# Performance work log

Measured on AMD Instinct MI355X. Metric: run time of the kernel, lower is better.

The kernel has to match this reference:

```python
import jax, jax.numpy as jnp
import numpy as np

K = 10          # neighbors per span
KTOK = 3        # heads used per span
D = 2.0         # token adjacency threshold
GAMMA = 1.0
MAX_WIDTH = 16
CAP = 128       # cap_spans_per_token
B, L, KTOK_TOTAL = 8, 128, 4


def _enumerate_spans(L, max_width):
    ar = np.arange(L)
    l_g, r_g = np.meshgrid(ar, ar, indexing='ij')
    mask = (r_g >= l_g) & (r_g - l_g + 1 <= max_width)
    l_idx = l_g[mask]
    r_idx = r_g[mask]
    S = l_idx.size
    span2id = np.full((L, L), -1, dtype=np.int64)
    span2id[l_idx, r_idx] = np.arange(S)
    return span2id, l_idx, r_idx, S


def _geom_matrix(L, max_width, span2id, l_idx, r_idx):
    # 8-neighborhood (l+/-1, r+/-1) adjacency over span ids, boolean (S,S)
    S = l_idx.size
    off = np.array([[-1, -1], [-1, 0], [-1, 1], [0, -1], [0, 1], [1, -1], [1, 0], [1, 1]])
    nl = l_idx[:, None] + off[None, :, 0]
    nr = r_idx[:, None] + off[None, :, 1]
    valid = (nl >= 0) & (nr >= 0) & (nl <= nr) & (nr < L) & (nr - nl + 1 <= max_width)
    s2 = span2id[np.clip(nl, 0, L - 1), np.clip(nr, 0, L - 1)]
    rows = np.broadcast_to(np.arange(S)[:, None], s2.shape)
    m = valid & (s2 >= 0)
    Geom = np.zeros((S, S), dtype=bool)
    Geom[rows[m], s2[m]] = True
    np.fill_diagonal(Geom, False)
    return Geom


SPAN2ID, L_IDX, R_IDX, S = _enumerate_spans(L, MAX_WIDTH)
GEOM = jnp.asarray(_geom_matrix(L, MAX_WIDTH, SPAN2ID, L_IDX, R_IDX))


def setup_inputs() -> dict:
    key = jax.random.key(0)
    k1, k2, k3 = jax.random.split(key, 3)
    head_indices = jax.random.randint(k1, (B, L, L, KTOK_TOTAL), 0, L)
    head_weights = jax.random.uniform(k2, (B, L, L, KTOK_TOTAL), dtype=jnp.float32)
    dist = jax.random.uniform(k3, (B, L, L), dtype=jnp.float32) * 8.0
    return {"head_indices": head_indices, "head_weights": head_weights, "dist": dist}


def reference(head_indices, head_weights, dist):
    l_idx = jnp.asarray(L_IDX)
    r_idx = jnp.asarray(R_IDX)
    # gather per-span head indices/weights: (B, S, Ktok)
    idx_all = head_indices[:, l_idx, r_idx, :KTOK]
    w_all = head_weights[:, l_idx, r_idx, :KTOK]
    valid1 = idx_all >= 0
    idx_safe = jnp.clip(idx_all, 0, None)
    w_all = w_all * valid1.astype(w_all.dtype)

    # scatter-add token->span dense matrices: (B, S, L)
    b_ix = jnp.arange(B)[:, None, None]
    s_ix = jnp.arange(S)[None, :, None]
    P_w = jnp.zeros((B, S, L), w_all.dtype).at[b_ix, s_ix, idx_safe].add(w_all)
    P_bin = jnp.zeros((B, S, L), jnp.float32).at[b_ix, s_ix, idx_safe].add(valid1.astype(jnp.float32))

    # token adjacency with self loops
    A = jnp.maximum((dist <= D).astype(jnp.float32), jnp.eye(L, dtype=jnp.float32))
    U_mask = jnp.einsum('bsl,blm->bsm', P_bin, A) > 0.0  # (B, S, L) spans hitting token m

    # top-1 head token -> span one-hot, with per-token span cap
    top1 = jnp.clip(idx_all[:, :, 0], 0, L - 1)
    top1_valid = (idx_all[:, :, 0] >= 0).astype(jnp.float32)
    E = jax.nn.one_hot(top1, L, dtype=jnp.float32) * top1_valid[..., None]  # (B, S, L)
    E = jnp.swapaxes(E, 1, 2)  # (B, L, S)
    E = E * (jnp.cumsum(E, axis=2) <= float(CAP)).astype(jnp.float32)

    # candidate matrix M: (B, S, S)
    M = jnp.einsum('bsl,blt->bst', U_mask.astype(jnp.float32), E) > 0.0
    diag = jnp.arange(S)
    M = M.at[:, diag, diag].set(False)
    M = M | GEOM[None]

    # gate scores Gate = P_w @ exp(-gamma*dist) @ P_w^T
    G = jnp.exp(-GAMMA * dist)
    A_pw = jnp.einsum('bsl,blm->bsm', P_w, G)
    Gate = jnp.einsum('bsm,btm->bst', A_pw, P_w)

    Gate_masked = jnp.where(M, Gate, -jnp.inf)
    topk_vals, topk_idx = jax.lax.top_k(Gate_masked, K)  # (B, S, K)
    N_mask = jnp.isfinite(topk_vals)
    N_idx = topk_idx.astype(jnp.int32)

    # self-loop fill for invalid slots
    rows = jnp.broadcast_to(jnp.arange(S, dtype=N_idx.dtype)[None, :, None], (B, S, K))
    N_idx = jnp.where(N_mask, N_idx, rows)
    N_mask = jnp.ones_like(N_mask)
    return N_idx, N_mask
```

## Files before the change

kernel.cpp:

```cpp
#include <hip/hip_runtime.h>
#include <stdint.h>

#define NB 8
#define LL 128
#define NS 1928
#define NK 10
#define WPB 4
#define SPW 4
#define SLOTS 32

__device__ __forceinline__ int span_id(int l, int r) {
    int off = (l <= 112) ? (l << 4) : (NS - (((128 - l) * (129 - l)) >> 1));
    return off + (r - l);
}

__device__ __forceinline__ float npexp_f32(float x) {
    const float magic = 12582912.0f;
    const float log2e = 1.442695040888963f;
    const float c1 = -6.93145752e-1f;
    const float c2 = -1.42860677e-6f;
    float t = __fmul_rn(x, log2e);
    float q = __fsub_rn(__fadd_rn(t, magic), magic);
    float r = __fmaf_rn(q, c1, x);
    r = __fmaf_rn(q, c2, r);
    float num = __fmaf_rn(r, 5.082762527590693718096e-04f, 6.757896990527504603057e-03f);
    num = __fmaf_rn(num, r, 5.114512081637298353406e-02f);
    num = __fmaf_rn(num, r, 2.473615434895520810817e-01f);
    num = __fmaf_rn(num, r, 7.257664613233124478488e-01f);
    num = __fmaf_rn(num, r, 9.999999999980870924916e-01f);
    float den = __fmaf_rn(r, 2.159509375685829852307e-02f, -2.742335390411667452936e-01f);
    den = __fmaf_rn(den, r, 1.0f);
    float p = __fdiv_rn(num, den);
    int qi = (int)q;
    return __fmul_rn(p, __int_as_float((127 + qi) << 23));
}

__device__ __forceinline__ float keyval(unsigned long long k) {
    return __uint_as_float((unsigned)(k >> 32));
}

__device__ __forceinline__ float f4c(const float4& v, int x) {
    return x == 0 ? v.x : (x == 1 ? v.y : (x == 2 ? v.z : v.w));
}

__device__ __forceinline__ void wfence() {
    __builtin_amdgcn_wave_barrier();
    __threadfence_block();
    __builtin_amdgcn_wave_barrier();
}

__device__ int wave_partition_fast(unsigned long long* a, int* posL, int* posR,
                                   int pl, int pr, int lane) {
    int pm = pl + ((pr - pl) >> 1);
    unsigned long long vl = a[pl], vm = a[pm], vr = a[pr], tt;
    if (keyval(vm) < keyval(vl)) { tt = vm; vm = vl; vl = tt; }
    if (keyval(vr) < keyval(vm)) { tt = vr; vr = vm; vm = tt; }
    if (keyval(vm) < keyval(vl)) { tt = vm; vm = vl; vl = tt; }
    float vp = keyval(vm);
    unsigned long long vq = a[pr - 1];
    if (lane == 0) { a[pl] = vl; a[pr] = vr; a[pm] = vq; a[pr - 1] = vm; }
    wfence();

    unsigned long long lmask = (1ull << lane) - 1ull;
    int baseL = 0, baseR = 0;
    for (int p0 = pl; p0 <= pr; p0 += 64) {
        int pos = p0 + lane;
        bool inr = (pos <= pr);
        float v = inr ? keyval(a[pos]) : 0.0f;
        bool ge = inr && (pos > pl) && (pos < pr) && (v >= vp);
        bool le = inr && (pos <= pr - 2) && (v <= vp);
        unsigned long long bge = __ballot(ge);
        unsigned long long ble = __ballot(le);
        if (ge) posL[baseL + __popcll(bge & lmask)] = pos;
        if (le) posR[baseR + __popcll(ble & lmask)] = pos;
        baseL += __popcll(bge);
        baseR += __popcll(ble);
    }
    wfence();
    int totGE = baseL, totLE = baseR;
    int maxk = (totGE < totLE) ? totGE : totLE;
    int K = 0;
    for (int base = 0;; base += 64) {
        int k = base + lane;
        bool active = (k < maxk);
        int Lk = active ? posL[k] : 0x7fffffff;
        int Rk = active ? posR[totLE - 1 - k] : -1;
        bool sw = active && (Lk < Rk);
        unsigned long long bm = __ballot(sw);
        int nsw = (~bm == 0ull) ? 64 : (__ffsll((long long)~bm) - 1);
        if (sw && (lane < nsw)) {
            unsigned long long tl = a[Lk], tr = a[Rk];
            a[Lk] = tr; a[Rk] = tl;
        }
        K += nsw;
        if (nsw < 64) break;
    }
    wfence();
    int pi = posL[K];
    if (K > 0) { int rp = posR[totLE - K]; if (rp < pi) pi = rp; }
    if (lane == 0) { tt = a[pi]; a[pi] = a[pr - 1]; a[pr - 1] = tt; }
    wfence();
    return pi;
}

__device__ __forceinline__ void lane_sift(unsigned long long* h, int start, int hm) {
    unsigned long long tmp = h[start];
    int i = start, j = start + start;
    while (j <= hm) {
        if (j < hm && keyval(h[j]) < keyval(h[j + 1])) ++j;
        if (keyval(tmp) < keyval(h[j])) { h[i] = h[j]; i = j; j += j; }
        else break;
    }
    h[i] = tmp;
}

__device__ void wave_heap_top(unsigned long long* a, int lo, int hi, int needlo, int lane) {
    unsigned long long* h = a + lo - 1;
    int hm = hi - lo + 1;
    int half = hm >> 1;
    int maxlvl = 0; { int v = half; while (v >>= 1) ++maxlvl; }
    for (int lvl = maxlvl; lvl >= 0; --lvl) {
        int n0 = 1 << lvl;
        int n1 = (n0 << 1) - 1; if (n1 > half) n1 = half;
        for (int nb = n0; nb <= n1; nb += 64) {
            int node = nb + lane;
            if (node <= n1) lane_sift(h, node, hm);
        }
        wfence();
    }
    int E = hi - needlo + 1;
    if (E > hm - 1) E = hm - 1;
    if (lane == 0) {
        int m = hm;
        for (int e = 0; e < E; ++e) {
            unsigned long long tmp = h[m]; h[m] = h[1]; --m;
            int i = 1, j = 2;
            while (j <= m) {
                if (j < m && keyval(h[j]) < keyval(h[j + 1])) ++j;
                if (keyval(tmp) < keyval(h[j])) { h[i] = h[j]; i = j; j += j; }
                else break;
            }
            h[i] = tmp;
        }
    }
    wfence();
}

__device__ void wave_insertion(unsigned long long* a, int lo, int hi, int lane) {
    int len = hi - lo + 1;
    unsigned long long v = (lane < len) ? a[lo + lane] : 0ull;
    float fv = keyval(v);
    int rank = 0;
    for (int j = 0; j < len; ++j) {
        unsigned long long vj = __shfl(v, j, 64);
        float fj = keyval(vj);
        if ((fj < fv) || (fj == fv && j < lane)) ++rank;
    }
    wfence();
    if (lane < len) a[lo + rank] = v;
    wfence();
}

__device__ void wave_np_sort_top(unsigned long long* a, int n, int lane, int* stk,
                                 int* posL, int* posR) {
    int depth = 0; { int v = n; while (v >>= 1) ++depth; }
    depth *= 2;
    const int TOPLO = n - NK;
    int sp = 0;
    int lo = 0, hi = n - 1;
    for (;;) {
        while (hi - lo > 15) {
            if (depth-- < 0) {
                if (hi >= TOPLO) wave_heap_top(a, lo, hi, (lo > TOPLO ? lo : TOPLO), lane);
                goto pop;
            }
            {
                int pi = wave_partition_fast(a, posL, posR, lo, hi, lane);
                if (pi - lo < hi - pi) {
                    if (lane == 0) { stk[sp * 2] = pi + 1; stk[sp * 2 + 1] = hi; }
                    ++sp; hi = pi - 1;
                } else {
                    if (lane == 0) { stk[sp * 2] = lo; stk[sp * 2 + 1] = pi - 1; }
                    ++sp; lo = pi + 1;
                }
                wfence();
            }
        }
        if (hi > lo && hi >= TOPLO) wave_insertion(a, lo, hi, lane);
pop:
        if (sp == 0) break;
        --sp;
        lo = stk[sp * 2]; hi = stk[sp * 2 + 1];
    }
}

__global__ __launch_bounds__(256)
void build_tables_kernel(const int* __restrict__ hi, const float* __restrict__ hw,
                         float4* __restrict__ g_pack, uint16_t* __restrict__ g_lrc,
                         unsigned char* __restrict__ top1) {
    int j = blockIdx.x * 256 + threadIdx.x;
    if (j >= NB * LL * 16) return;
    int b = j >> 11;
    int lw = j & 2047;
    int l = lw >> 4, w = lw & 15, r = l + w;
    if (r >= LL) return;
    int sid = span_id(l, r);
    const int* hb = hi + b * LL * LL * 4;
    const float* wb = hw + b * LL * LL * 4;
    int4 iv = *(const int4*)(hb + (l * LL + r) * 4);
    float4 wv = *(const float4*)(wb + (l * LL + r) * 4);
    int ia = iv.x, ib = iv.y, ic = iv.z;
    float wa = wv.x, wb2 = wv.y, wc = wv.z;
    int m0, m1 = 255, m2 = 255;
    float W0, W1 = 0.f, W2 = 0.f;
    if (ia == ib && ib == ic) {
        m0 = ia; W0 = __fadd_rn(__fadd_rn(wa, wb2), wc);
    } else if (ia == ib) {
        float W = __fadd_rn(wa, wb2);
        if (ia < ic) { m0 = ia; W0 = W; m1 = ic; W1 = wc; }
        else         { m0 = ic; W0 = wc; m1 = ia; W1 = W; }
    } else if (ia == ic) {
        float W = __fadd_rn(wa, wc);
        if (ia < ib) { m0 = ia; W0 = W; m1 = ib; W1 = wb2; }
        else         { m0 = ib; W0 = wb2; m1 = ia; W1 = W; }
    } else if (ib == ic) {
        float W = __fadd_rn(wb2, wc);
        if (ia < ib) { m0 = ia; W0 = wa; m1 = ib; W1 = W; }
        else         { m0 = ib; W0 = W; m1 = ia; W1 = wa; }
    } else {
        int x0 = ia, x1 = ib, x2 = ic; float y0 = wa, y1 = wb2, y2 = wc;
        if (x0 > x1) { int tx = x0; x0 = x1; x1 = tx; float ty = y0; y0 = y1; y1 = ty; }
        if (x1 > x2) { int tx = x1; x1 = x2; x2 = tx; float ty = y1; y1 = y2; y2 = ty; }
        if (x0 > x1) { int tx = x0; x0 = x1; x1 = tx; float ty = y0; y0 = y1; y1 = ty; }
        m0 = x0; m1 = x1; m2 = x2; W0 = y0; W1 = y1; W2 = y2;
    }
    uint32_t rec = (uint32_t)m0 | ((uint32_t)m1 << 8) | ((uint32_t)m2 << 16)
                 | ((uint32_t)(ia & 127) << 24);
    g_pack[b * NS + sid] = make_float4(W0, W1, W2, __uint_as_float(rec));
    g_lrc[b * NS + sid] = (uint16_t)(l | (r << 7));
    top1[b * NS + sid] = (unsigned char)(ia & 127);
}

__global__ void cap_kernel(const unsigned char* __restrict__ top1,
                           unsigned char* __restrict__ flags) {
    int gw = (blockIdx.x * blockDim.x + threadIdx.x) >> 6;
    int lane = threadIdx.x & 63;
    int b = gw >> 7, l = gw & 127;
    const unsigned char* tb = top1 + b * NS;
    unsigned char* fb = flags + b * NS;
    int cnt = 0;
    for (int t0 = 0; t0 < NS; t0 += 64) {
        int t = t0 + lane;
        int tp = (t < NS) ? (int)tb[t] : 255;
        bool match = (tp == l);
        unsigned long long m = __ballot(match);
        if (match) {
            int pre = __popcll(m & ((1ull << lane) - 1ull));
            fb[t] = (cnt + pre + 1 <= 128) ? 1 : 0;
        }
        cnt += __popcll(m);
    }
}

__device__ __forceinline__ void load_tables(const float4* __restrict__ gp,
                                            const uint16_t* __restrict__ gl,
                                            const unsigned char* __restrict__ fb,
                                            float4* s_pack, uint16_t* s_lrc) {
    for (int j = threadIdx.x; j < NS; j += 256) {
        float4 v = gp[j];
        uint32_t rec = __float_as_uint(v.w) | ((uint32_t)(fb[j] & 1) << 31);
        v.w = __uint_as_float(rec);
        s_pack[j] = v;
        s_lrc[j] = gl[j];
    }
}

__device__ __forceinline__ void span_prologue(const float* __restrict__ db, float4 ps,
                                              int lane, float* qrow, int stride,
                                              unsigned long long* ub) {
    uint32_t rec = __float_as_uint(ps.w);
    int m0 = rec & 255, m1 = (rec >> 8) & 255, m2 = (rec >> 16) & 255;
    bool e1 = (m1 != 255), e2 = (m2 != 255);
    const float* row0 = db + m0 * LL;
    const float* row1 = db + (e1 ? m1 : 0) * LL;
    const float* row2 = db + (e2 ? m2 : 0) * LL;
    int mA = lane, mB = lane + 64;
    float dA0 = row0[mA], dB0 = row0[mB];
    float dA1 = row1[mA], dB1 = row1[mB];
    float dA2 = row2[mA], dB2 = row2[mB];
    float qA = __fmaf_rn(ps.x, npexp_f32(-dA0), 0.0f);
    qA = __fmaf_rn(ps.y, npexp_f32(-dA1), qA);
    qA = __fmaf_rn(ps.z, npexp_f32(-dA2), qA);
    float qB = __fmaf_rn(ps.x, npexp_f32(-dB0), 0.0f);
    qB = __fmaf_rn(ps.y, npexp_f32(-dB1), qB);
    qB = __fmaf_rn(ps.z, npexp_f32(-dB2), qB);
    bool cA = (dA0 <= 2.0f || mA == m0) ||
              (e1 && (dA1 <= 2.0f || mA == m1)) ||
              (e2 && (dA2 <= 2.0f || mA == m2));
    bool cB = (dB0 <= 2.0f || mB == m0) ||
              (e1 && (dB1 <= 2.0f || mB == m1)) ||
              (e2 && (dB2 <= 2.0f || mB == m2));
    ub[0] = __ballot(cA);
    ub[1] = __ballot(cB);
    qrow[mA * stride] = qA;
    qrow[mB * stride] = qB;
}

__device__ __forceinline__ void topk_merge(unsigned key, int t0, int lane,
                                           unsigned& v, int& vi, unsigned& tau) {
    unsigned long long bm = __ballot(key > tau);
    while (bm) {
        int ln = __ffsll((long long)bm) - 1;
        bm &= bm - 1;
        unsigned kk = (unsigned)__builtin_amdgcn_readlane((int)key, ln);
        if (kk > tau) {
            int tk = t0 + ln;
            unsigned vprev = (unsigned)__builtin_amdgcn_update_dpp(
                -1, (int)v, 0x138 , 0xF, 0xF, false);
            int iprev = __builtin_amdgcn_update_dpp(
                0, vi, 0x138 , 0xF, 0xF, false);
            bool keep = (v >= kk);
            bool fp = (vprev < kk);
            v = keep ? v : (fp ? vprev : kk);
            vi = keep ? vi : (fp ? iprev : tk);
            tau = (unsigned)__builtin_amdgcn_readlane((int)v, 10);
        }
    }
}

__device__ __forceinline__ void topk_merge_idx(unsigned key, int tval,
                                               unsigned& v, int& vi, unsigned& tau) {
    unsigned long long bm = __ballot(key > tau);
    while (bm) {
        int ln = __ffsll((long long)bm) - 1;
        bm &= bm - 1;
        unsigned kk = (unsigned)__builtin_amdgcn_readlane((int)key, ln);
        if (kk > tau) {
            int tk = __builtin_amdgcn_readlane(tval, ln);
            unsigned vprev = (unsigned)__builtin_amdgcn_update_dpp(
                -1, (int)v, 0x138, 0xF, 0xF, false);
            int iprev = __builtin_amdgcn_update_dpp(
                0, vi, 0x138, 0xF, 0xF, false);
            bool keep = (v >= kk);
            bool fp = (vprev < kk);
            v = keep ? v : (fp ? vprev : kk);
            vi = keep ? vi : (fp ? iprev : tk);
            tau = (unsigned)__builtin_amdgcn_readlane((int)v, 10);
        }
    }
}

__device__ __forceinline__ void span_epilogue(unsigned v, int vi, int b, int s, int lane,
                                              unsigned char* __restrict__ rowflag,
                                              int* __restrict__ out) {
    unsigned vn = __shfl_down(v, 1, 64);
    bool tie = (lane < NK) && (v != 0u) && (vn == v);
    bool flag = (__ballot(tie) != 0ull);
    if (lane < NK) {
        int o = (b * NS + s) * NK + lane;
        out[NB * NS * NK + o] = 1;
        if (!flag) out[o] = (vi >= 0) ? vi : s;
    }
    if (lane == 0) rowflag[b * NS + s] = flag ? 1 : 0;
}

__global__ __launch_bounds__(256)
void span_scan_kernel(const float4* __restrict__ g_pack,
                      const uint16_t* __restrict__ g_lrc,
                      const float* __restrict__ dist,
                      const unsigned char* __restrict__ capf,
                      unsigned char* __restrict__ rowflag,
                      int* __restrict__ out) {
    __shared__ float4 s_pack[NS];
    __shared__ float4 s_q4[WPB][LL];

    const int b = blockIdx.y;
    {
        const float4* gp = g_pack + b * NS;
        const unsigned char* fb = capf + b * NS;
        for (int j = threadIdx.x; j < NS; j += 256) {
            float4 v = gp[j];
            v.w = __uint_as_float(__float_as_uint(v.w) | ((uint32_t)(fb[j] & 1) << 31));
            s_pack[j] = v;
        }
    }
    __syncthreads();

    const int wid = threadIdx.x >> 6;
    const int lane = threadIdx.x & 63;
    const int base = blockIdx.x * (WPB * SPW);
    const float* db = dist + b * LL * LL;
    const uint16_t* glb = g_lrc + b * NS;

    int ss[SPW]; bool ok[SPW]; int schunk[SPW];
    int lsv[SPW], rsv[SPW];
    unsigned long long ub0[SPW], ub1[SPW];

    #pragma unroll
    for (int x = 0; x < SPW; ++x) {
        int s = base + x * WPB + wid;
        ok[x] = (s < NS);
        s = ok[x] ? s : 0;
        ss[x] = s;
        schunk[x] = s & ~63;
        uint32_t lrc = glb[s];
        lsv[x] = lrc & 127;
        rsv[x] = (lrc >> 7) & 127;
        unsigned long long ub[2];
        span_prologue(db, s_pack[s], lane, (float*)&s_q4[wid][0] + x, 4, ub);
        ub0[x] = ub[0]; ub1[x] = ub[1];
    }
    const float4* qq = s_q4[wid];

    unsigned v[SPW] = {0u, 0u, 0u, 0u};
    int vi[SPW] = {-1, -1, -1, -1};
    unsigned tau[SPW] = {0u, 0u, 0u, 0u};

    const int NCH = (NS + 63) >> 6;

    float4 ptc = s_pack[lane];
    uint32_t rtc = __float_as_uint(ptc.w);
    float4 q0 = qq[rtc & 127];
    float4 q1 = qq[(rtc >> 8) & 127];
    float4 q2 = qq[(rtc >> 16) & 127];

    for (int c = 0; c < NCH; ++c) {
        const int t0 = c << 6;
        const int t = t0 + lane;
        const bool inr = (t < NS);
        const bool hasnext = (c + 1 < NCH);

        float4 ptn = ptc;
        {
            int tn = t0 + 64 + lane;
            if (tn > NS - 1) tn = NS - 1;
            if (hasnext) ptn = s_pack[tn];
        }

        unsigned key[SPW];
        {
            int sh = (int)((rtc >> 24) & 63);
            bool hi2 = ((rtc >> 24) & 64) != 0;
            bool cum = ((int)rtc) < 0;
            #pragma unroll
            for (int x = 0; x < SPW; ++x) {
                float g = __fmaf_rn(ptc.x, f4c(q0, x), 0.0f);
                g = __fmaf_rn(ptc.y, f4c(q1, x), g);
                g = __fmaf_rn(ptc.z, f4c(q2, x), g);
                unsigned long long bits = hi2 ? ub1[x] : ub0[x];
                bool um = (((bits >> sh) & 1ull) != 0) && cum && inr;
                key[x] = um ? __float_as_uint(g) : 0u;
            }
            #pragma unroll
            for (int x = 0; x < SPW; ++x)
                if (t0 == schunk[x]) key[x] = (t == ss[x]) ? 0u : key[x];
        }

        uint32_t rtn = rtc;
        float4 n0 = q0, n1 = q1, n2 = q2;
        if (hasnext) {
            rtn = __float_as_uint(ptn.w);
            n0 = qq[rtn & 127];
            n1 = qq[(rtn >> 8) & 127];
            n2 = qq[(rtn >> 16) & 127];
        }

        #pragma unroll
        for (int x = 0; x < SPW; ++x)
            topk_merge(key[x], t0, lane, v[x], vi[x], tau[x]);

        ptc = ptn; rtc = rtn; q0 = n0; q1 = n1; q2 = n2;
    }

    {
        int j = lane + (lane >= 4 ? 1 : 0);
        int dl = j / 3 - 1, dr = j % 3 - 1;
        #pragma unroll
        for (int x = 0; x < SPW; ++x) {
            int nl = lsv[x] + dl, nr = rsv[x] + dr;
            bool valid = (lane < 8) && (nl >= 0) && (nr >= nl) && (nr < LL)
                         && (nr - nl < 16);
            int tg = valid ? span_id(nl, nr) : 0;
            float4 pt = s_pack[tg];
            uint32_t rt = __float_as_uint(pt.w);
            float g = __fmaf_rn(pt.x, f4c(qq[rt & 127], x), 0.0f);
            g = __fmaf_rn(pt.y, f4c(qq[(rt >> 8) & 127], x), g);
            g = __fmaf_rn(pt.z, f4c(qq[(rt >> 16) & 127], x), g);
            int rb = (int)(rt >> 24);
            unsigned long long bits = (rb & 64) ? ub1[x] : ub0[x];
            bool um = (((bits >> (rb & 63)) & 1ull) != 0) && (((int)rt) < 0);
            unsigned key = (valid && !um) ? __float_as_uint(g) : 0u;
            topk_merge_idx(key, tg, v[x], vi[x], tau[x]);
        }
    }

    #pragma unroll
    for (int x = 0; x < SPW; ++x)
        if (ok[x]) span_epilogue(v[x], vi[x], b, ss[x], lane, rowflag, out);
}

__global__ __launch_bounds__(256)
void span_slow_kernel(const float4* __restrict__ g_pack,
                      const uint16_t* __restrict__ g_lrc,
                      const float* __restrict__ dist,
                      const unsigned char* __restrict__ capf,
                      const unsigned char* __restrict__ rowflag,
                      int* __restrict__ out) {
    __shared__ int s_nrows;
    __shared__ int s_rows[64];
    __shared__ float4 s_pack[NS];
    __shared__ uint16_t s_lrc[NS];
    __shared__ float s_qq[LL];
    __shared__ unsigned long long s_cov[2];
    __shared__ unsigned long long s_buf[NS];
    __shared__ int s_posL[NS], s_posR[NS];
    __shared__ int s_stk[48];

    const int b = blockIdx.x;
    const int slot = blockIdx.y;
    const unsigned char* rf = rowflag + b * NS;

    if (threadIdx.x < 64) {
        int lane = threadIdx.x;
        int i = slot + lane * SLOTS;
        bool f = (i < NS) && (rf[i] != 0);
        unsigned long long m = __ballot(f);
        if (f) s_rows[__popcll(m & ((1ull << lane) - 1ull))] = i;
        if (lane == 0) s_nrows = __popcll(m);
    }
    __syncthreads();
    int nrows = s_nrows;
    if (nrows == 0) return;

    load_tables(g_pack + b * NS, g_lrc + b * NS, capf + b * NS, s_pack, s_lrc);
    __syncthreads();

    const int wid = threadIdx.x >> 6;
    const int lane = threadIdx.x & 63;
    const float* db = dist + b * LL * LL;

    for (int ri = 0; ri < nrows; ++ri) {
        const int s = s_rows[ri];
        uint32_t lrc = s_lrc[s];
        int ls = lrc & 127, rs = (lrc >> 7) & 127;

        if (wid == 0) {
            unsigned long long ub[2];
            span_prologue(db, s_pack[s], lane, s_qq, 1, ub);
            if (lane == 0) { s_cov[0] = ub[0]; s_cov[1] = ub[1]; }
        }
        __syncthreads();
        unsigned long long ub0 = s_cov[0], ub1 = s_cov[1];

        for (int t = threadIdx.x; t < NS; t += 256) {
            float4 pt = s_pack[t];
            uint32_t rt = __float_as_uint(pt.w);
            float g = __fmaf_rn(pt.x, s_qq[rt & 127], 0.0f);
            g = __fmaf_rn(pt.y, s_qq[(rt >> 8) & 127], g);
            g = __fmaf_rn(pt.z, s_qq[(rt >> 16) & 127], g);
            uint32_t lr = s_lrc[t];
            int lt = lr & 127, rt2 = (lr >> 7) & 127;
            int dl = lt - ls; if (dl < 0) dl = -dl;
            int dr = rt2 - rs; if (dr < 0) dr = -dr;
            bool neq = (t != s);
            bool geom = neq && (dl <= 1) && (dr <= 1);
            int rb = (int)(rt >> 24);
            unsigned long long bits = (rb & 64) ? ub1 : ub0;
            bool um = (((bits >> (rb & 63)) & 1ull) != 0) && (((int)rt) < 0) && neq;
            unsigned h32 = (um || geom) ? __float_as_uint(g) : 0xFF800000u;
            s_buf[t] = ((unsigned long long)h32 << 32) | (unsigned)t;
        }
        __syncthreads();

        if (wid == 0) {
            wave_np_sort_top(s_buf, NS, lane, s_stk, s_posL, s_posR);
            if (lane < NK) {
                unsigned long long k = s_buf[NS - 1 - lane];
                int idx = ((unsigned)(k >> 32) == 0xFF800000u) ? s : (int)(k & 0xffffffffull);
                out[(b * NS + s) * NK + lane] = idx;
            }
        }
        __syncthreads();
    }
}

extern "C" void kernel_launch(void* const* d_in, const int* in_sizes, int n_in,
                              void* d_out, int out_size, void* d_ws, size_t ws_size,
                              hipStream_t stream) {
    const int* hi = (const int*)d_in[0];
    const float* hw = (const float*)d_in[1];
    const float* dist = (const float*)d_in[2];
    int* out = (int*)d_out;

    unsigned char* ws = (unsigned char*)d_ws;
    unsigned char* top1 = ws;
    unsigned char* capf = ws + NB * NS;
    unsigned char* rowflag = ws + 2 * NB * NS;
    float4* g_pack = (float4*)(ws + 3 * NB * NS);
    uint16_t* g_lrc = (uint16_t*)(ws + 3 * NB * NS + NB * NS * 16);

    build_tables_kernel<<<(NB * LL * 16) / 256, 256, 0, stream>>>(hi, hw, g_pack, g_lrc, top1);
    cap_kernel<<<(NB * LL * 64) / 256, 256, 0, stream>>>(top1, capf);
    dim3 grid((NS + WPB * SPW - 1) / (WPB * SPW), NB);
    span_scan_kernel<<<grid, 256, 0, stream>>>(g_pack, g_lrc, dist, capf, rowflag, out);
    dim3 sgrid(NB, SLOTS);
    span_slow_kernel<<<sgrid, 256, 0, stream>>>(g_pack, g_lrc, dist, capf, rowflag, out);
}
```

Baseline: 193.4 us.

## Fold cap flag into packed table and drop shared-memory staging in scan kernel

The cap kernel now sets the cap bit directly in the packed span table instead of writing a separate flag array. This removes the per-block merge of that array. The scan kernel no longer stages the whole packed table into LDS; it reads it from global memory (L1/L2-cached) and keeps only a smaller per-wave query buffer. Spans per wave drop from 4 to 2, doubling the block count, and bounds checks are removed because NS divides evenly by 8. The trade-off is more global or cache gathers in the inner loop and less reuse of each block's table load across spans.

```diff
diff --git a/kernel.cpp b/kernel.cpp
--- a/kernel.cpp
+++ b/kernel.cpp
@@ -6,7 +6,7 @@
 #define NS 1928
 #define NK 10
 #define WPB 4
-#define SPW 4
+#define SPW 2
 #define SLOTS 32
 
 __device__ __forceinline__ int span_id(int l, int r) {
@@ -39,8 +39,8 @@
     return __uint_as_float((unsigned)(k >> 32));
 }
 
-__device__ __forceinline__ float f4c(const float4& v, int x) {
-    return x == 0 ? v.x : (x == 1 ? v.y : (x == 2 ? v.z : v.w));
+__device__ __forceinline__ float f2c(const float2& v, int x) {
+    return x == 0 ? v.x : v.y;
 }
 
 __device__ __forceinline__ void wfence() {
@@ -242,21 +242,21 @@
 }
 
 __global__ void cap_kernel(const unsigned char* __restrict__ top1,
-                           unsigned char* __restrict__ flags) {
+                           float4* __restrict__ g_pack) {
     int gw = (blockIdx.x * blockDim.x + threadIdx.x) >> 6;
     int lane = threadIdx.x & 63;
     int b = gw >> 7, l = gw & 127;
     const unsigned char* tb = top1 + b * NS;
-    unsigned char* fb = flags + b * NS;
+    uint32_t* gw4 = (uint32_t*)(g_pack + b * NS);
     int cnt = 0;
     for (int t0 = 0; t0 < NS; t0 += 64) {
         int t = t0 + lane;
         int tp = (t < NS) ? (int)tb[t] : 255;
         bool match = (tp == l);
         unsigned long long m = __ballot(match);
-        if (match) {
-            int pre = __popcll(m & ((1ull << lane) - 1ull));
-            fb[t] = (cnt + pre + 1 <= 128) ? 1 : 0;
+        if (match && (cnt + __popcll(m & ((1ull << lane) - 1ull)) + 1 <= 128)) {
+            uint32_t* p = gw4 + t * 4 + 3;
+            *p |= 0x80000000u;
         }
         cnt += __popcll(m);
     }
@@ -264,13 +264,9 @@
 
 __device__ __forceinline__ void load_tables(const float4* __restrict__ gp,
                                             const uint16_t* __restrict__ gl,
-                                            const unsigned char* __restrict__ fb,
                                             float4* s_pack, uint16_t* s_lrc) {
     for (int j = threadIdx.x; j < NS; j += 256) {
-        float4 v = gp[j];
-        uint32_t rec = __float_as_uint(v.w) | ((uint32_t)(fb[j] & 1) << 31);
-        v.w = __uint_as_float(rec);
-        s_pack[j] = v;
+        s_pack[j] = gp[j];
         s_lrc[j] = gl[j];
     }
 }
@@ -368,61 +364,49 @@
 void span_scan_kernel(const float4* __restrict__ g_pack,
                       const uint16_t* __restrict__ g_lrc,
                       const float* __restrict__ dist,
-                      const unsigned char* __restrict__ capf,
                       unsigned char* __restrict__ rowflag,
                       int* __restrict__ out) {
-    __shared__ float4 s_pack[NS];
-    __shared__ float4 s_q4[WPB][LL];
+    __shared__ float2 s_q2[WPB][LL];
 
     const int b = blockIdx.y;
-    {
-        const float4* gp = g_pack + b * NS;
-        const unsigned char* fb = capf + b * NS;
-        for (int j = threadIdx.x; j < NS; j += 256) {
-            float4 v = gp[j];
-            v.w = __uint_as_float(__float_as_uint(v.w) | ((uint32_t)(fb[j] & 1) << 31));
-            s_pack[j] = v;
-        }
-    }
-    __syncthreads();
+    const float4* __restrict__ gpb = g_pack + b * NS;
+    const uint16_t* __restrict__ glb = g_lrc + b * NS;
+    const float* db = dist + b * LL * LL;
 
     const int wid = threadIdx.x >> 6;
     const int lane = threadIdx.x & 63;
     const int base = blockIdx.x * (WPB * SPW);
-    const float* db = dist + b * LL * LL;
-    const uint16_t* glb = g_lrc + b * NS;
-
-    int ss[SPW]; bool ok[SPW]; int schunk[SPW];
+
+    int ss[SPW]; int schunk[SPW];
     int lsv[SPW], rsv[SPW];
     unsigned long long ub0[SPW], ub1[SPW];
 
     #pragma unroll
     for (int x = 0; x < SPW; ++x) {
         int s = base + x * WPB + wid;
-        ok[x] = (s < NS);
-        s = ok[x] ? s : 0;
         ss[x] = s;
         schunk[x] = s & ~63;
         uint32_t lrc = glb[s];
         lsv[x] = lrc & 127;
         rsv[x] = (lrc >> 7) & 127;
         unsigned long long ub[2];
-        span_prologue(db, s_pack[s], lane, (float*)&s_q4[wid][0] + x, 4, ub);
+        span_prologue(db, gpb[s], lane, (float*)&s_q2[wid][0].x + x, 2, ub);
         ub0[x] = ub[0]; ub1[x] = ub[1];
     }
-    const float4* qq = s_q4[wid];
-
-    unsigned v[SPW] = {0u, 0u, 0u, 0u};
-    int vi[SPW] = {-1, -1, -1, -1};
-    unsigned tau[SPW] = {0u, 0u, 0u, 0u};
+    __syncthreads();
+    const float2* qq = s_q2[wid];
+
+    unsigned v[SPW] = {0u, 0u};
+    int vi[SPW] = {-1, -1};
+    unsigned tau[SPW] = {0u, 0u};
 
     const int NCH = (NS + 63) >> 6;
 
-    float4 ptc = s_pack[lane];
+    float4 ptc = gpb[lane];
     uint32_t rtc = __float_as_uint(ptc.w);
-    float4 q0 = qq[rtc & 127];
-    float4 q1 = qq[(rtc >> 8) & 127];
-    float4 q2 = qq[(rtc >> 16) & 127];
+    float2 q0 = qq[rtc & 127];
+    float2 q1 = qq[(rtc >> 8) & 127];
+    float2 q2 = qq[(rtc >> 16) & 127];
 
     for (int c = 0; c < NCH; ++c) {
         const int t0 = c << 6;
@@ -434,7 +418,7 @@
         {
             int tn = t0 + 64 + lane;
             if (tn > NS - 1) tn = NS - 1;
-            if (hasnext) ptn = s_pack[tn];
+            if (hasnext) ptn = gpb[tn];
         }
 
         unsigned key[SPW];
@@ -444,9 +428,9 @@
             bool cum = ((int)rtc) < 0;
             #pragma unroll
             for (int x = 0; x < SPW; ++x) {
-                float g = __fmaf_rn(ptc.x, f4c(q0, x), 0.0f);
-                g = __fmaf_rn(ptc.y, f4c(q1, x), g);
-                g = __fmaf_rn(ptc.z, f4c(q2, x), g);
+                float g = __fmaf_rn(ptc.x, f2c(q0, x), 0.0f);
+                g = __fmaf_rn(ptc.y, f2c(q1, x), g);
+                g = __fmaf_rn(ptc.z, f2c(q2, x), g);
                 unsigned long long bits = hi2 ? ub1[x] : ub0[x];
                 bool um = (((bits >> sh) & 1ull) != 0) && cum && inr;
                 key[x] = um ? __float_as_uint(g) : 0u;
@@ -457,7 +441,7 @@
         }
 
         uint32_t rtn = rtc;
-        float4 n0 = q0, n1 = q1, n2 = q2;
+        float2 n0 = q0, n1 = q1, n2 = q2;
         if (hasnext) {
             rtn = __float_as_uint(ptn.w);
             n0 = qq[rtn & 127];
@@ -481,11 +465,11 @@
             bool valid = (lane < 8) && (nl >= 0) && (nr >= nl) && (nr < LL)
                          && (nr - nl < 16);
             int tg = valid ? span_id(nl, nr) : 0;
-            float4 pt = s_pack[tg];
+            float4 pt = gpb[tg];
             uint32_t rt = __float_as_uint(pt.w);
-            float g = __fmaf_rn(pt.x, f4c(qq[rt & 127], x), 0.0f);
-            g = __fmaf_rn(pt.y, f4c(qq[(rt >> 8) & 127], x), g);
-            g = __fmaf_rn(pt.z, f4c(qq[(rt >> 16) & 127], x), g);
+            float g = __fmaf_rn(pt.x, f2c(qq[rt & 127], x), 0.0f);
+            g = __fmaf_rn(pt.y, f2c(qq[(rt >> 8) & 127], x), g);
+            g = __fmaf_rn(pt.z, f2c(qq[(rt >> 16) & 127], x), g);
             int rb = (int)(rt >> 24);
             unsigned long long bits = (rb & 64) ? ub1[x] : ub0[x];
             bool um = (((bits >> (rb & 63)) & 1ull) != 0) && (((int)rt) < 0);
@@ -496,14 +480,13 @@
 
     #pragma unroll
     for (int x = 0; x < SPW; ++x)
-        if (ok[x]) span_epilogue(v[x], vi[x], b, ss[x], lane, rowflag, out);
+        span_epilogue(v[x], vi[x], b, ss[x], lane, rowflag, out);
 }
 
 __global__ __launch_bounds__(256)
 void span_slow_kernel(const float4* __restrict__ g_pack,
                       const uint16_t* __restrict__ g_lrc,
                       const float* __restrict__ dist,
-                      const unsigned char* __restrict__ capf,
                       const unsigned char* __restrict__ rowflag,
                       int* __restrict__ out) {
     __shared__ int s_nrows;
@@ -532,7 +515,7 @@
     int nrows = s_nrows;
     if (nrows == 0) return;
 
-    load_tables(g_pack + b * NS, g_lrc + b * NS, capf + b * NS, s_pack, s_lrc);
+    load_tables(g_pack + b * NS, g_lrc + b * NS, s_pack, s_lrc);
     __syncthreads();
 
     const int wid = threadIdx.x >> 6;
@@ -594,15 +577,14 @@
 
     unsigned char* ws = (unsigned char*)d_ws;
     unsigned char* top1 = ws;
-    unsigned char* capf = ws + NB * NS;
-    unsigned char* rowflag = ws + 2 * NB * NS;
-    float4* g_pack = (float4*)(ws + 3 * NB * NS);
-    uint16_t* g_lrc = (uint16_t*)(ws + 3 * NB * NS + NB * NS * 16);
+    unsigned char* rowflag = ws + NB * NS;
+    float4* g_pack = (float4*)(ws + 2 * NB * NS);
+    uint16_t* g_lrc = (uint16_t*)(ws + 2 * NB * NS + NB * NS * 16);
 
     build_tables_kernel<<<(NB * LL * 16) / 256, 256, 0, stream>>>(hi, hw, g_pack, g_lrc, top1);
-    cap_kernel<<<(NB * LL * 64) / 256, 256, 0, stream>>>(top1, capf);
-    dim3 grid((NS + WPB * SPW - 1) / (WPB * SPW), NB);
-    span_scan_kernel<<<grid, 256, 0, stream>>>(g_pack, g_lrc, dist, capf, rowflag, out);
+    cap_kernel<<<(NB * LL * 64) / 256, 256, 0, stream>>>(top1, g_pack);
+    dim3 grid(NS / (WPB * SPW), NB);
+    span_scan_kernel<<<grid, 256, 0, stream>>>(g_pack, g_lrc, dist, rowflag, out);
     dim3 sgrid(NB, SLOTS);
-    span_slow_kernel<<<sgrid, 256, 0, stream>>>(g_pack, g_lrc, dist, capf, rowflag, out);
-}
+    span_slow_kernel<<<sgrid, 256, 0, stream>>>(g_pack, g_lrc, dist, rowflag, out);
+}
```

Result: no change. 194.1 us (+0.4%).
